# Kernel optimization log

Hardware: AMD Instinct MI355X
Metric: run time of the kernel (lower is better)

Reference implementation:

```python
import jax, jax.numpy as jnp
import numpy as np
from jax.ops import segment_sum, segment_max

N = 100000   # nodes
E = 1600000  # edges
B = 256      # graphs
H = 128      # hidden_channels
F_IN = 4     # input_size
EPS = 1e-5


def _graph_norm(x, w, b, ms, batch):
    # PyG GraphNorm: out = w * (x - ms*mean_g) / sqrt(var_g + eps) + b
    cnt = jnp.maximum(segment_sum(jnp.ones((x.shape[0],), x.dtype), batch, num_segments=B), 1.0)
    mean = segment_sum(x, batch, num_segments=B) / cnt[:, None]
    out = x - mean[batch] * ms
    var = segment_sum(out * out, batch, num_segments=B) / cnt[:, None]
    return w * out / jnp.sqrt(var + EPS)[batch] + b


def _gcn(x, W, b, src, dst):
    # GCNConv with self-loops and symmetric normalization (src/dst already include self-loops)
    h = x @ W                                              # [N, H]
    deg = segment_sum(jnp.ones_like(src, dtype=h.dtype), dst, num_segments=N)
    dinv = jax.lax.rsqrt(jnp.maximum(deg, 1.0))
    norm = dinv[src] * dinv[dst]                           # [E+N]
    return segment_sum(norm[:, None] * h[src], dst, num_segments=N) + b


def _seg_softmax(gate, batch):
    gmax = segment_max(gate, batch, num_segments=B)
    e = jnp.exp(gate - gmax[batch])
    den = segment_sum(e, batch, num_segments=B)
    return e / den[batch]


def setup_inputs() -> dict:
    key = jax.random.key(0)
    ks = jax.random.split(key, 16)
    x = jax.random.normal(ks[0], (N, F_IN), jnp.float32)
    edge_index = jax.random.randint(ks[1], (2, E), 0, N, dtype=jnp.int64)
    batch = jnp.sort(jax.random.randint(ks[2], (N,), 0, B, dtype=jnp.int64))
    r = lambda k, shp, fan: jax.random.normal(k, shp, jnp.float32) / np.sqrt(fan)
    inp = {
        "x": x, "edge_index": edge_index, "batch": batch,
        "W1": r(ks[3], (F_IN, H), F_IN), "b1": jnp.zeros((H,), jnp.float32),
        "W2": r(ks[4], (H, H), H), "b2": jnp.zeros((H,), jnp.float32),
        "W3": r(ks[5], (H, H), H), "b3": jnp.zeros((H,), jnp.float32),
        "gn0_w": jnp.ones((F_IN,), jnp.float32), "gn0_b": jnp.zeros((F_IN,), jnp.float32), "gn0_ms": jnp.ones((F_IN,), jnp.float32),
        "gn1_w": jnp.ones((H,), jnp.float32), "gn1_b": jnp.zeros((H,), jnp.float32), "gn1_ms": jnp.ones((H,), jnp.float32),
        "gn2_w": jnp.ones((H,), jnp.float32), "gn2_b": jnp.zeros((H,), jnp.float32), "gn2_ms": jnp.ones((H,), jnp.float32),
        "gn3_w": jnp.ones((H,), jnp.float32), "gn3_b": jnp.zeros((H,), jnp.float32), "gn3_ms": jnp.ones((H,), jnp.float32),
        "g1": r(ks[6], (H, H), H), "gb1": jnp.zeros((H,), jnp.float32),
        "g2": r(ks[7], (H, H), H), "gb2": jnp.zeros((H,), jnp.float32),
        "g3": r(ks[8], (H, 1), H), "gb3": jnp.zeros((1,), jnp.float32),
        "l1": r(ks[9], (H, H), H), "lb1": jnp.zeros((H,), jnp.float32),
        "l2": r(ks[10], (H, H), H), "lb2": jnp.zeros((H,), jnp.float32),
        "l3": r(ks[11], (H, 1), H), "lb3": jnp.zeros((1,), jnp.float32),
    }
    return inp


def reference(x, edge_index, batch, W1, b1, W2, b2, W3, b3,
              gn0_w, gn0_b, gn0_ms, gn1_w, gn1_b, gn1_ms,
              gn2_w, gn2_b, gn2_ms, gn3_w, gn3_b, gn3_ms,
              g1, gb1, g2, gb2, g3, gb3,
              l1, lb1, l2, lb2, l3, lb3):
    loop = jnp.arange(N, dtype=edge_index.dtype)
    src = jnp.concatenate([edge_index[0], loop])
    dst = jnp.concatenate([edge_index[1], loop])

    h = _graph_norm(x, gn0_w, gn0_b, gn0_ms, batch)
    h = _gcn(h, W1, b1, src, dst)
    h = jax.nn.relu(_graph_norm(h, gn1_w, gn1_b, gn1_ms, batch))
    h = _gcn(h, W2, b2, src, dst)
    h = jax.nn.relu(_graph_norm(h, gn2_w, gn2_b, gn2_ms, batch))
    h = _gcn(h, W3, b3, src, dst)
    h = _graph_norm(h, gn3_w, gn3_b, gn3_ms, batch)

    # GlobalAttention: gate_nn -> scalar gate per node, segment softmax, weighted sum
    g = jax.nn.relu(h @ g1 + gb1)
    g = jax.nn.relu(g @ g2 + gb2)
    gate = g @ g3 + gb3                                   # [N, 1]
    attn = _seg_softmax(gate, batch)                      # [N, 1]
    pooled = segment_sum(attn * h, batch, num_segments=B) # [B, H]

    o = jax.nn.relu(pooled @ l1 + lb1)
    o = jax.nn.relu(o @ l2 + lb2)
    return o @ l3 + lb3                                   # [B, 1]
```

## Files before the change

### kernel.cpp

```cpp
#include <hip/hip_runtime.h>
#include <hip/hip_bf16.h>

#define NN 100000
#define NE 1600000
#define NB 256
#define HD 128
#define EPS 1e-5f
#define NBUK 1563
#define EPB 8192
#define NCHK 8

typedef __attribute__((ext_vector_type(8))) short bf16x8v;
typedef __attribute__((ext_vector_type(4))) float f32x4v;

__device__ __forceinline__ float rd_dyn(const void* p, int i, int fflag) {
    if (fflag) {
        unsigned short u = ((const unsigned short*)p)[i];
        return __uint_as_float(((unsigned)u) << 16);
    }
    return ((const float*)p)[i];
}

__device__ __forceinline__ int rd_idx(const int* p, int k, int iflag) {
    return iflag ? p[k] : p[2 * k];
}

__device__ __forceinline__ unsigned short f2bf(float v) {
    __hip_bfloat16 b = __float2bfloat16(v);
    return *(unsigned short*)&b;
}

__device__ __forceinline__ float bflo(unsigned u) { return __uint_as_float(u << 16); }
__device__ __forceinline__ float bfhi(unsigned u) { return __uint_as_float(u & 0xFFFF0000u); }
__device__ __forceinline__ unsigned packbf(float a, float b) {
    return (unsigned)f2bf(a) | ((unsigned)f2bf(b) << 16);
}

__global__ void k_zeroi(int* __restrict__ p, int n) {
    int i = blockIdx.x * blockDim.x + threadIdx.x;
    if (i < n) p[i] = 0;
}

__global__ void k_mark7(unsigned short* __restrict__ out, int n) {
    int i = blockIdx.x * blockDim.x + threadIdx.x;
    if (i < n) out[i] = 0x40E0;
}

__global__ void k_init(const unsigned* __restrict__ w, int* __restrict__ flags) {
    if (threadIdx.x == 0 && blockIdx.x == 0) {
        flags[0] = 0;
        flags[1] = (w[0] == 0x3F803F80u) ? 1 : 0;
    }
}

__global__ void k_detect(const int* __restrict__ w, int* __restrict__ iflag, int n) {
    int i = blockIdx.x * blockDim.x + threadIdx.x;
    if (i < n && (i & 1) && w[i] != 0) atomicOr(iflag, 1);
}

struct CvtArgs {
    const void* p[30];
    int n[30];
    int off[30];
};
__global__ void k_cvtf_all(CvtArgs a, float* __restrict__ out, const int* __restrict__ fflagp) {
    int j = blockIdx.y;
    int i = blockIdx.x * blockDim.x + threadIdx.x;
    if (i >= a.n[j]) return;
    out[a.off[j] + i] = rd_dyn(a.p[j], i, *fflagp);
}

__global__ void k_transp(const float* __restrict__ P, int o0, int o1, int o2, int o3,
                         unsigned short* __restrict__ WT) {
    int mat = blockIdx.y;
    int off = mat == 0 ? o0 : mat == 1 ? o1 : mat == 2 ? o2 : o3;
    int i = blockIdx.x * 256 + threadIdx.x;
    int nidx = i >> 7, k = i & 127;
    WT[mat * 16384 + nidx * 128 + k] = f2bf(P[off + k * 128 + nidx]);
}

__global__ __launch_bounds__(256) void k_bhist(const int* __restrict__ ei,
                                               const int* __restrict__ iflagp,
                                               int* __restrict__ bcnt, int e) {
    __shared__ int lh[NBUK];
    int ifl = *iflagp;
    for (int b = threadIdx.x; b < NBUK; b += 256) lh[b] = 0;
    __syncthreads();
    int s0 = blockIdx.x * EPB;
    int s1 = s0 + EPB; if (s1 > e) s1 = e;
    for (int i = s0 + threadIdx.x; i < s1; i += 256) {
        int d = rd_idx(ei, NE + i, ifl);
        int s = rd_idx(ei, i, ifl);
        if ((unsigned)d < (unsigned)NN && (unsigned)s < (unsigned)NN)
            atomicAdd(&lh[d >> 6], 1);
    }
    __syncthreads();
    for (int b = threadIdx.x; b < NBUK; b += 256)
        if (lh[b]) atomicAdd(&bcnt[b], lh[b]);
}

__global__ __launch_bounds__(1024) void k_bscan(const int* __restrict__ bcnt,
                                                int* __restrict__ boff,
                                                int* __restrict__ bcur) {
    __shared__ int part[1024];
    int t = threadIdx.x;
    int i0 = t * 2;
    int a = (i0 < NBUK) ? bcnt[i0] : 0;
    int b = (i0 + 1 < NBUK) ? bcnt[i0 + 1] : 0;
    part[t] = a + b;
    __syncthreads();
    for (int off = 1; off < 1024; off <<= 1) {
        int add = (t >= off) ? part[t - off] : 0;
        __syncthreads();
        part[t] += add;
        __syncthreads();
    }
    int base = (t > 0) ? part[t - 1] : 0;
    if (i0 < NBUK) { boff[i0] = base; bcur[i0] = base; }
    if (i0 + 1 < NBUK) { boff[i0 + 1] = base + a; bcur[i0 + 1] = base + a; }
    if (t == 1023) boff[NBUK] = part[1023];
}

__global__ __launch_bounds__(256) void k_bfill(const int* __restrict__ ei,
                                               const int* __restrict__ iflagp,
                                               int* __restrict__ bcur,
                                               unsigned* __restrict__ bkte, int e) {
    __shared__ int lh[NBUK];
    __shared__ int lbase[NBUK];
    int ifl = *iflagp;
    for (int b = threadIdx.x; b < NBUK; b += 256) lh[b] = 0;
    __syncthreads();
    int s0 = blockIdx.x * EPB;
    int s1 = s0 + EPB; if (s1 > e) s1 = e;
    for (int i = s0 + threadIdx.x; i < s1; i += 256) {
        int d = rd_idx(ei, NE + i, ifl);
        int s = rd_idx(ei, i, ifl);
        if ((unsigned)d < (unsigned)NN && (unsigned)s < (unsigned)NN)
            atomicAdd(&lh[d >> 6], 1);
    }
    __syncthreads();
    for (int b = threadIdx.x; b < NBUK; b += 256) {
        int c = lh[b];
        if (c) { lbase[b] = atomicAdd(&bcur[b], c); lh[b] = 0; }
    }
    __syncthreads();
    for (int i = s0 + threadIdx.x; i < s1; i += 256) {
        int d = rd_idx(ei, NE + i, ifl);
        int s = rd_idx(ei, i, ifl);
        if ((unsigned)d < (unsigned)NN && (unsigned)s < (unsigned)NN) {
            int b = d >> 6;
            int li = atomicAdd(&lh[b], 1);
            bkte[lbase[b] + li] = ((unsigned)s << 6) | (unsigned)(d & 63);
        }
    }
}

__global__ __launch_bounds__(256) void k_csrfin(const unsigned* __restrict__ bkte,
                                                const int* __restrict__ boff,
                                                int* __restrict__ rowptr,
                                                int* __restrict__ cnt,
                                                float* __restrict__ dinv,
                                                int* __restrict__ esrc) {
    __shared__ int lc[64];
    __shared__ int lcur[64];
    int b = blockIdx.x, t = threadIdx.x;
    int base = b * 64;
    if (t < 64) lc[t] = 0;
    __syncthreads();
    int r0 = boff[b], r1 = boff[b + 1];
    for (int j = r0 + t; j < r1; j += 256)
        atomicAdd(&lc[(int)(bkte[j] & 63u)], 1);
    __syncthreads();
    if (t < 64) {
        int v = lc[t];
        int inc = v;
#pragma unroll
        for (int off = 1; off < 64; off <<= 1) {
            int nv = __shfl_up(inc, off, 64);
            if (t >= off) inc += nv;
        }
        int ex = r0 + inc - v;
        lcur[t] = ex;
        int node = base + t;
        if (node < NN) {
            rowptr[node] = ex;
            cnt[node] = v;
            dinv[node] = rsqrtf((float)(v + 1));
        }
    }
    __syncthreads();
    for (int j = r0 + t; j < r1; j += 256) {
        unsigned p = bkte[j];
        int slot = atomicAdd(&lcur[p & 63u], 1);
        esrc[slot] = (int)(p >> 6);
    }
}

__global__ void k_start(const int* __restrict__ batch, const int* __restrict__ iflagp,
                        int* __restrict__ start, int* __restrict__ batch32, int n) {
    int i = blockIdx.x * blockDim.x + threadIdx.x;
    if (i >= n) return;
    int ifl = *iflagp;
    int b = rd_idx(batch, i, ifl); b = b < 0 ? 0 : (b > NB - 1 ? NB - 1 : b);
    batch32[i] = b;
    int bp;
    if (i == 0) bp = -1;
    else { bp = rd_idx(batch, i - 1, ifl); bp = bp < 0 ? 0 : (bp > NB - 1 ? NB - 1 : bp); }
    for (int g = bp + 1; g <= b; ++g) start[g] = i;
    if (i == n - 1) { for (int g = b + 1; g <= NB; ++g) start[g] = n; }
}

__global__ __launch_bounds__(64) void k_gn4(const void* __restrict__ x,
                                            const float* __restrict__ w,
                                            const float* __restrict__ bb,
                                            const float* __restrict__ ms,
                                            const int* __restrict__ start,
                                            const int* __restrict__ fflagp,
                                            float* __restrict__ out) {
    int g = blockIdx.x;
    int s0 = start[g], s1 = start[g + 1];
    if (s1 <= s0) return;
    int ff = *fflagp;
    float cnt = (float)(s1 - s0);
    int t = threadIdx.x;
    int c = t & 3, p = t >> 2;
    __shared__ float reds[64], redq[64];
    float s = 0.f, q = 0.f;
    for (int n = s0 + p; n < s1; n += 16) {
        float v = rd_dyn(x, n * 4 + c, ff);
        s += v; q = fmaf(v, v, q);
    }
    reds[t] = s; redq[t] = q; __syncthreads();
    for (int off = 8; off >= 1; off >>= 1) {
        if (p < off) { reds[t] += reds[t + 4 * off]; redq[t] += redq[t + 4 * off]; }
        __syncthreads();
    }
    float mean = reds[c] / cnt;
    float sq = redq[c] / cnt;
    float sub = mean * ms[c];
    float var = sq - 2.f * sub * mean + sub * sub;
    float scale = w[c] * rsqrtf(var + EPS);
    float bias = bb[c];
    for (int n = s0 + p; n < s1; n += 16) {
        float d = rd_dyn(x, n * 4 + c, ff) - sub;
        out[n * 4 + c] = scale * d + bias;
    }
}

__global__ __launch_bounds__(256) void k_gnstats_part(const unsigned* __restrict__ Xu,
                                                      const int* __restrict__ start,
                                                      float* __restrict__ PS,
                                                      float* __restrict__ PQ) {
    int g = blockIdx.x, k = blockIdx.y;
    int s0 = start[g], s1 = start[g + 1];
    int len = (s1 - s0 + NCHK - 1) / NCHK;
    int c0 = s0 + k * len, c1 = c0 + len; if (c1 > s1) c1 = s1;
    int t = threadIdx.x;
    int cp = t & 63, p = t >> 6;
    __shared__ float r0s[256], r1s[256], r0q[256], r1q[256];
    float s0a = 0.f, s1a = 0.f, q0a = 0.f, q1a = 0.f;
    for (int n = c0 + p; n < c1; n += 4) {
        unsigned u = Xu[n * 64 + cp];
        float lo = bflo(u), hi = bfhi(u);
        s0a += lo; q0a = fmaf(lo, lo, q0a);
        s1a += hi; q1a = fmaf(hi, hi, q1a);
    }
    r0s[t] = s0a; r1s[t] = s1a; r0q[t] = q0a; r1q[t] = q1a;
    __syncthreads();
    if (p == 0) {
        float a0 = r0s[cp] + r0s[64 + cp] + r0s[128 + cp] + r0s[192 + cp];
        float a1 = r1s[cp] + r1s[64 + cp] + r1s[128 + cp] + r1s[192 + cp];
        float b0 = r0q[cp] + r0q[64 + cp] + r0q[128 + cp] + r0q[192 + cp];
        float b1 = r1q[cp] + r1q[64 + cp] + r1q[128 + cp] + r1q[192 + cp];
        int bidx = (g * NCHK + k) * 128;
        PS[bidx + 2 * cp] = a0; PS[bidx + 2 * cp + 1] = a1;
        PQ[bidx + 2 * cp] = b0; PQ[bidx + 2 * cp + 1] = b1;
    }
}

__global__ __launch_bounds__(128) void k_gnstats_final(const float* __restrict__ PS,
                                                       const float* __restrict__ PQ,
                                                       const float* __restrict__ w,
                                                       const float* __restrict__ ms,
                                                       const int* __restrict__ start,
                                                       float* __restrict__ SUB,
                                                       float* __restrict__ SCALE) {
    int g = blockIdx.x, c = threadIdx.x;
    int n = start[g + 1] - start[g];
    if (n <= 0) return;
    float cnt = (float)n;
    float s = 0.f, q = 0.f;
#pragma unroll
    for (int k = 0; k < NCHK; ++k) {
        s += PS[(g * NCHK + k) * 128 + c];
        q += PQ[(g * NCHK + k) * 128 + c];
    }
    float mean = s / cnt;
    float sq = q / cnt;
    float sub = mean * ms[c];
    float var = sq - 2.f * sub * mean + sub * sub;
    SUB[g * 128 + c] = sub;
    SCALE[g * 128 + c] = w[c] * rsqrtf(var + EPS);
}

__global__ __launch_bounds__(256) void k_gather4(const int* __restrict__ rowptr,
                                                 const int* __restrict__ cnt,
                                                 const int* __restrict__ esrc,
                                                 const float* __restrict__ dinv,
                                                 const float* __restrict__ h,
                                                 float* __restrict__ out) {
    int node = blockIdx.x * blockDim.x + threadIdx.x;
    if (node >= NN) return;
    int r0 = rowptr[node], r1 = r0 + cnt[node];
    const float4* h4 = (const float4*)h;
    double ax = 0.0, ay = 0.0, az = 0.0, aw = 0.0;
    for (int j = r0; j < r1; ++j) {
        int s = esrc[j];
        float ds = dinv[s];
        float4 v = h4[s];
        ax += (double)(ds * v.x); ay += (double)(ds * v.y);
        az += (double)(ds * v.z); aw += (double)(ds * v.w);
    }
    float dd = dinv[node];
    float4 hs = h4[node];
    float4 o;
    o.x = (float)(dd * ax) + dd * dd * hs.x;
    o.y = (float)(dd * ay) + dd * dd * hs.y;
    o.z = (float)(dd * az) + dd * dd * hs.z;
    o.w = (float)(dd * aw) + dd * dd * hs.w;
    ((float4*)out)[node] = o;
}

__global__ __launch_bounds__(256) void k_gemm4b(const float* __restrict__ in,
                                                const float* __restrict__ W,
                                                const float* __restrict__ bias,
                                                unsigned short* __restrict__ out) {
    __shared__ float xs[16][4];
    int base = blockIdx.x * 16;
    int tid = threadIdx.x;
    if (tid < 64) xs[tid >> 2][tid & 3] = in[base * 4 + tid];
    __syncthreads();
    int j = tid & 127;
    int half = tid >> 7;
    float w0 = W[0 * HD + j], w1 = W[1 * HD + j], w2 = W[2 * HD + j], w3 = W[3 * HD + j];
    float bj = bias[j];
#pragma unroll
    for (int r = 0; r < 8; ++r) {
        int row = half * 8 + r;
        float v = xs[row][0] * w0 + xs[row][1] * w1 + xs[row][2] * w2 + xs[row][3] * w3 + bj;
        out[(base + row) * HD + j] = f2bf(v);
    }
}

__global__ __launch_bounds__(256) void k_gemm_mfma_bf(const unsigned* __restrict__ Xu,
                                                      const int* __restrict__ batch32,
                                                      const float* __restrict__ SUB,
                                                      const float* __restrict__ SCALE,
                                                      const float* __restrict__ gnb,
                                                      int relu,
                                                      const unsigned short* __restrict__ WT,
                                                      const float* __restrict__ dinv,
                                                      unsigned short* __restrict__ out) {
    __shared__ unsigned short xs[16][136];
    int base = blockIdx.x * 16;
    int tid = threadIdx.x;
    for (int idx = tid; idx < 1024; idx += 256) {
        int r = idx >> 6, cp = idx & 63;
        int g = batch32[base + r];
        unsigned u = Xu[(base + r) * 64 + cp];
        int ca = 2 * cp, cb = 2 * cp + 1;
        float va = (bflo(u) - SUB[g * 128 + ca]) * SCALE[g * 128 + ca] + gnb[ca];
        float vb = (bfhi(u) - SUB[g * 128 + cb]) * SCALE[g * 128 + cb] + gnb[cb];
        if (relu) { va = fmaxf(va, 0.f); vb = fmaxf(vb, 0.f); }
        xs[r][ca] = f2bf(va);
        xs[r][cb] = f2bf(vb);
    }
    __syncthreads();
    int wave = tid >> 6, lane = tid & 63;
    int m = lane & 15, quad = lane >> 4;
    f32x4v acc0 = {0.f, 0.f, 0.f, 0.f}, acc1 = {0.f, 0.f, 0.f, 0.f};
    int c0 = wave * 32 + m, c1 = c0 + 16;
#pragma unroll
    for (int kk = 0; kk < 4; ++kk) {
        int ko = kk * 32 + quad * 8;
        bf16x8v a  = *(const bf16x8v*)&xs[m][ko];
        bf16x8v b0 = *(const bf16x8v*)&WT[c0 * 128 + ko];
        bf16x8v b1 = *(const bf16x8v*)&WT[c1 * 128 + ko];
        acc0 = __builtin_amdgcn_mfma_f32_16x16x32_bf16(a, b0, acc0, 0, 0, 0);
        acc1 = __builtin_amdgcn_mfma_f32_16x16x32_bf16(a, b1, acc1, 0, 0, 0);
    }
#pragma unroll
    for (int reg = 0; reg < 4; ++reg) {
        int row = base + quad * 4 + reg;
        float dv = dinv[row];
        out[row * 128 + c0] = f2bf(dv * acc0[reg]);
        out[row * 128 + c1] = f2bf(dv * acc1[reg]);
    }
}

__global__ __launch_bounds__(256) void k_gather_bf(const int* __restrict__ rowptr,
                                                   const int* __restrict__ cnt,
                                                   const int* __restrict__ esrc,
                                                   const float* __restrict__ dinv,
                                                   const unsigned* __restrict__ h,
                                                   const float* __restrict__ bias,
                                                   unsigned* __restrict__ Xu) {
    int node = blockIdx.x * 4 + (threadIdx.x >> 6);
    int lane = threadIdx.x & 63;
    if (node >= NN) return;
    int r0 = rowptr[node], r1 = r0 + cnt[node];
    double ax = 0.0, ay = 0.0;
    int j = r0;
    for (; j + 7 < r1; j += 8) {
        unsigned u[8];
#pragma unroll
        for (int q = 0; q < 8; ++q) u[q] = h[esrc[j + q] * 64 + lane];
#pragma unroll
        for (int q = 0; q < 8; ++q) {
            ax += (double)bflo(u[q]);
            ay += (double)bfhi(u[q]);
        }
    }
    for (; j < r1; ++j) {
        unsigned u = h[esrc[j] * 64 + lane];
        ax += (double)bflo(u);
        ay += (double)bfhi(u);
    }
    float dd = dinv[node];
    unsigned us = h[node * 64 + lane];
    float2 bb = ((const float2*)bias)[lane];
    float ox = dd * ((float)ax + bflo(us)) + bb.x;
    float oy = dd * ((float)ay + bfhi(us)) + bb.y;
    Xu[node * 64 + lane] = packbf(ox, oy);
}

__global__ __launch_bounds__(256) void k_gate_fused(const unsigned* __restrict__ Xu,
                                                    const int* __restrict__ batch32,
                                                    const float* __restrict__ SUB,
                                                    const float* __restrict__ SCALE,
                                                    const float* __restrict__ gnb,
                                                    const unsigned short* __restrict__ GT1,
                                                    const float* __restrict__ gb1,
                                                    const unsigned short* __restrict__ GT2,
                                                    const float* __restrict__ gb2,
                                                    const float* __restrict__ g3,
                                                    const float* __restrict__ gb3,
                                                    float* __restrict__ gate) {
    __shared__ unsigned short xs[16][136];
    __shared__ unsigned short t1[16][136];
    __shared__ float redw[64];
    int base = blockIdx.x * 16;
    int tid = threadIdx.x;
    for (int idx = tid; idx < 1024; idx += 256) {
        int r = idx >> 6, cp = idx & 63;
        int g = batch32[base + r];
        unsigned u = Xu[(base + r) * 64 + cp];
        int ca = 2 * cp, cb = 2 * cp + 1;
        xs[r][ca] = f2bf((bflo(u) - SUB[g * 128 + ca]) * SCALE[g * 128 + ca] + gnb[ca]);
        xs[r][cb] = f2bf((bfhi(u) - SUB[g * 128 + cb]) * SCALE[g * 128 + cb] + gnb[cb]);
    }
    __syncthreads();
    int wave = tid >> 6, lane = tid & 63;
    int m = lane & 15, quad = lane >> 4;
    int c0 = wave * 32 + m, c1 = c0 + 16;
    f32x4v acc0 = {0.f, 0.f, 0.f, 0.f}, acc1 = {0.f, 0.f, 0.f, 0.f};
#pragma unroll
    for (int kk = 0; kk < 4; ++kk) {
        int ko = kk * 32 + quad * 8;
        bf16x8v a  = *(const bf16x8v*)&xs[m][ko];
        bf16x8v b0 = *(const bf16x8v*)&GT1[c0 * 128 + ko];
        bf16x8v b1 = *(const bf16x8v*)&GT1[c1 * 128 + ko];
        acc0 = __builtin_amdgcn_mfma_f32_16x16x32_bf16(a, b0, acc0, 0, 0, 0);
        acc1 = __builtin_amdgcn_mfma_f32_16x16x32_bf16(a, b1, acc1, 0, 0, 0);
    }
    float bj0 = gb1[c0], bj1 = gb1[c1];
#pragma unroll
    for (int reg = 0; reg < 4; ++reg) {
        int row = quad * 4 + reg;
        t1[row][c0] = f2bf(fmaxf(acc0[reg] + bj0, 0.f));
        t1[row][c1] = f2bf(fmaxf(acc1[reg] + bj1, 0.f));
    }
    __syncthreads();
    f32x4v d0 = {0.f, 0.f, 0.f, 0.f}, d1 = {0.f, 0.f, 0.f, 0.f};
#pragma unroll
    for (int kk = 0; kk < 4; ++kk) {
        int ko = kk * 32 + quad * 8;
        bf16x8v a  = *(const bf16x8v*)&t1[m][ko];
        bf16x8v b0 = *(const bf16x8v*)&GT2[c0 * 128 + ko];
        bf16x8v b1 = *(const bf16x8v*)&GT2[c1 * 128 + ko];
        d0 = __builtin_amdgcn_mfma_f32_16x16x32_bf16(a, b0, d0, 0, 0, 0);
        d1 = __builtin_amdgcn_mfma_f32_16x16x32_bf16(a, b1, d1, 0, 0, 0);
    }
    float g30 = g3[c0], g31 = g3[c1];
    float bk0 = gb2[c0], bk1 = gb2[c1];
    float contrib[4];
#pragma unroll
    for (int reg = 0; reg < 4; ++reg) {
        float v0 = fmaxf(d0[reg] + bk0, 0.f);
        float v1 = fmaxf(d1[reg] + bk1, 0.f);
        contrib[reg] = v0 * g30 + v1 * g31;
    }
#pragma unroll
    for (int mask = 1; mask <= 8; mask <<= 1) {
#pragma unroll
        for (int reg = 0; reg < 4; ++reg)
            contrib[reg] += __shfl_xor(contrib[reg], mask, 64);
    }
    if (m == 0) {
#pragma unroll
        for (int reg = 0; reg < 4; ++reg)
            redw[wave * 16 + quad * 4 + reg] = contrib[reg];
    }
    __syncthreads();
    if (tid < 16) {
        float s = redw[tid] + redw[16 + tid] + redw[32 + tid] + redw[48 + tid];
        gate[base + tid] = s + gb3[0];
    }
}

__global__ __launch_bounds__(256) void k_softmax(float* __restrict__ gate,
                                                 const int* __restrict__ start) {
    int g = blockIdx.x;
    int s0 = start[g], s1 = start[g + 1];
    if (s1 <= s0) return;
    int t = threadIdx.x;
    __shared__ float red[256];
    float m = -1e30f;
    for (int i = s0 + t; i < s1; i += 256) m = fmaxf(m, gate[i]);
    red[t] = m; __syncthreads();
    for (int off = 128; off; off >>= 1) { if (t < off) red[t] = fmaxf(red[t], red[t + off]); __syncthreads(); }
    m = red[0]; __syncthreads();
    float s = 0.f;
    for (int i = s0 + t; i < s1; i += 256) s += expf(gate[i] - m);
    red[t] = s; __syncthreads();
    for (int off = 128; off; off >>= 1) { if (t < off) red[t] += red[t + off]; __syncthreads(); }
    float inv = 1.f / red[0];
    for (int i = s0 + t; i < s1; i += 256) gate[i] = expf(gate[i] - m) * inv;
}

__global__ __launch_bounds__(256) void k_pool_part(const unsigned* __restrict__ Xu,
                                                   const float* __restrict__ SUB,
                                                   const float* __restrict__ SCALE,
                                                   const float* __restrict__ gnb,
                                                   const float* __restrict__ attn,
                                                   const int* __restrict__ start,
                                                   float* __restrict__ PP) {
    int g = blockIdx.x, k = blockIdx.y;
    int s0 = start[g], s1 = start[g + 1];
    int len = (s1 - s0 + NCHK - 1) / NCHK;
    int c0 = s0 + k * len, c1 = c0 + len; if (c1 > s1) c1 = s1;
    int t = threadIdx.x, cp = t & 63, p = t >> 6;
    __shared__ float r0s[256], r1s[256];
    int ca = 2 * cp, cb = 2 * cp + 1;
    float suba = SUB[g * 128 + ca], subb = SUB[g * 128 + cb];
    float sca = SCALE[g * 128 + ca], scb = SCALE[g * 128 + cb];
    float ba = gnb[ca], bb2 = gnb[cb];
    float sa = 0.f, sb = 0.f;
    for (int n = c0 + p; n < c1; n += 4) {
        float a = attn[n];
        unsigned u = Xu[n * 64 + cp];
        sa += a * ((bflo(u) - suba) * sca + ba);
        sb += a * ((bfhi(u) - subb) * scb + bb2);
    }
    r0s[t] = sa; r1s[t] = sb; __syncthreads();
    if (p == 0) {
        int bidx = (g * NCHK + k) * 128;
        PP[bidx + ca] = r0s[cp] + r0s[64 + cp] + r0s[128 + cp] + r0s[192 + cp];
        PP[bidx + cb] = r1s[cp] + r1s[64 + cp] + r1s[128 + cp] + r1s[192 + cp];
    }
}

__global__ __launch_bounds__(128) void k_head(const float* __restrict__ PP,
                                              const float* __restrict__ l1, const float* __restrict__ lb1,
                                              const float* __restrict__ l2, const float* __restrict__ lb2,
                                              const float* __restrict__ l3, const float* __restrict__ lb3,
                                              const int* __restrict__ fflagp,
                                              void* __restrict__ out) {
    int g = blockIdx.x, t = threadIdx.x;
    __shared__ float p[128], o[128], red[128];
    float s = 0.f;
#pragma unroll
    for (int k = 0; k < NCHK; ++k) s += PP[(g * NCHK + k) * 128 + t];
    p[t] = s; __syncthreads();
    float a = 0.f;
    for (int k = 0; k < 128; ++k) a += p[k] * l1[k * 128 + t];
    a = fmaxf(a + lb1[t], 0.f);
    o[t] = a; __syncthreads();
    float b = 0.f;
    for (int k = 0; k < 128; ++k) b += o[k] * l2[k * 128 + t];
    b = fmaxf(b + lb2[t], 0.f);
    red[t] = b * l3[t]; __syncthreads();
    for (int off = 64; off; off >>= 1) { if (t < off) red[t] += red[t + off]; __syncthreads(); }
    if (t == 0) {
        float r = red[0] + lb3[0];
        if (*fflagp) ((__hip_bfloat16*)out)[g] = __float2bfloat16(r);
        else ((float*)out)[g] = r;
    }
}

extern "C" void kernel_launch(void* const* d_in, const int* in_sizes, int n_in,
                              void* d_out, int out_size, void* d_ws, size_t ws_size,
                              hipStream_t stream) {
    const void* x = d_in[0];
    const int* ei_raw = (const int*)d_in[1];
    const int* batch_raw = (const int*)d_in[2];
    (void)n_in; (void)out_size;

    char* ws = (char*)d_ws;
    size_t off = 0;
    auto alloc = [&](size_t bytes) -> void* {
        void* p = ws + off;
        off += (bytes + 255) & ~(size_t)255;
        return p;
    };
    unsigned* Xu  = (unsigned*)alloc((size_t)NN * HD * 2);
    float* Y      = (float*)alloc((size_t)NN * HD * 4);
    float* h0     = (float*)alloc((size_t)NN * 4 * 4);
    float* z4     = (float*)alloc((size_t)NN * 4 * 4);
    float* dinv   = (float*)alloc((size_t)NN * 4);
    float* gate   = (float*)alloc((size_t)NN * 4);
    int*   start  = (int*)alloc((size_t)(NB + 1) * 4);
    int*   batch32= (int*)alloc((size_t)NN * 4);
    float* P      = (float*)alloc((size_t)131072 * 4);
    unsigned short* WT = (unsigned short*)alloc((size_t)4 * 16384 * 2);
    float* SUB    = (float*)alloc((size_t)NB * HD * 4);
    float* SCALE  = (float*)alloc((size_t)NB * HD * 4);
    float* PS     = (float*)alloc((size_t)NB * NCHK * 128 * 4);
    float* PQ     = (float*)alloc((size_t)NB * NCHK * 128 * 4);
    int*   flags  = (int*)alloc(256);
    int*   cnt    = (int*)alloc((size_t)NN * 4);
    int*   rowptr = (int*)alloc((size_t)(NN + 1) * 4);
    int*   esrc   = (int*)alloc((size_t)NE * 4);
    int*   bcnt   = (int*)alloc((size_t)NBUK * 4);
    int*   boff   = (int*)alloc((size_t)(NBUK + 1) * 4);
    int*   bcur   = (int*)alloc((size_t)NBUK * 4);
    unsigned* bkte = (unsigned*)(Y + (size_t)NN * HD / 2);
    float* PP = PS;

    if (ws_size < off) {
        k_mark7<<<1, 256, 0, stream>>>((unsigned short*)d_out, NB);
        return;
    }

    int* iflag = flags;
    int* fflag = flags + 1;
    k_init<<<1, 64, 0, stream>>>((const unsigned*)d_in[12], flags);
    k_detect<<<(NN + 255) / 256, 256, 0, stream>>>(batch_raw, iflag, NN);

    CvtArgs ca;
    float* fp[33];
    int maxn = 1;
    {
        int poff = 0;
        for (int i = 3; i < 33; ++i) {
            int n = in_sizes[i];
            ca.p[i - 3] = d_in[i];
            ca.n[i - 3] = n;
            ca.off[i - 3] = poff;
            fp[i] = P + poff;
            poff += n;
            if (n > maxn) maxn = n;
        }
    }
    {
        dim3 grid((maxn + 255) / 256, 30);
        k_cvtf_all<<<grid, 256, 0, stream>>>(ca, P, fflag);
    }
    const float *W1 = fp[3], *b1 = fp[4], *b2 = fp[6], *b3 = fp[8];
    const float *gn0w = fp[9],  *gn0b = fp[10], *gn0m = fp[11];
    const float *gn1w = fp[12], *gn1b = fp[13], *gn1m = fp[14];
    const float *gn2w = fp[15], *gn2b = fp[16], *gn2m = fp[17];
    const float *gn3w = fp[18], *gn3b = fp[19], *gn3m = fp[20];
    const float *gb1 = fp[22], *gb2 = fp[24], *g3 = fp[25], *gb3 = fp[26];
    const float *l1 = fp[27], *lb1 = fp[28], *l2 = fp[29], *lb2 = fp[30], *l3 = fp[31], *lb3 = fp[32];

    {
        dim3 grid(64, 4);
        k_transp<<<grid, 256, 0, stream>>>(P, (int)(fp[5] - P), (int)(fp[7] - P),
                                           (int)(fp[21] - P), (int)(fp[23] - P), WT);
    }
    const unsigned short* WT2 = WT;
    const unsigned short* WT3 = WT + 16384;
    const unsigned short* GT1 = WT + 2 * 16384;
    const unsigned short* GT2 = WT + 3 * 16384;

    k_start<<<(NN + 255) / 256, 256, 0, stream>>>(batch_raw, iflag, start, batch32, NN);

    int ebg = (NE + EPB - 1) / EPB;
    k_zeroi<<<(NBUK + 255) / 256, 256, 0, stream>>>(bcnt, NBUK);
    k_bhist<<<ebg, 256, 0, stream>>>(ei_raw, iflag, bcnt, NE);
    k_bscan<<<1, 1024, 0, stream>>>(bcnt, boff, bcur);
    k_bfill<<<ebg, 256, 0, stream>>>(ei_raw, iflag, bcur, bkte, NE);
    k_csrfin<<<NBUK, 256, 0, stream>>>(bkte, boff, rowptr, cnt, dinv, esrc);

    k_gn4<<<NB, 64, 0, stream>>>(x, gn0w, gn0b, gn0m, start, fflag, h0);

    k_gather4<<<(NN + 255) / 256, 256, 0, stream>>>(rowptr, cnt, esrc, dinv, h0, z4);
    k_gemm4b<<<NN / 16, 256, 0, stream>>>(z4, W1, b1, (unsigned short*)Xu);

    unsigned short* Yb = (unsigned short*)Y;
    dim3 sgrid(NB, NCHK);

    k_gnstats_part<<<sgrid, 256, 0, stream>>>(Xu, start, PS, PQ);
    k_gnstats_final<<<NB, 128, 0, stream>>>(PS, PQ, gn1w, gn1m, start, SUB, SCALE);
    k_gemm_mfma_bf<<<NN / 16, 256, 0, stream>>>(Xu, batch32, SUB, SCALE, gn1b, 1, WT2, dinv, Yb);
    k_gather_bf<<<(NN + 3) / 4, 256, 0, stream>>>(rowptr, cnt, esrc, dinv, (const unsigned*)Yb, b2, Xu);

    k_gnstats_part<<<sgrid, 256, 0, stream>>>(Xu, start, PS, PQ);
    k_gnstats_final<<<NB, 128, 0, stream>>>(PS, PQ, gn2w, gn2m, start, SUB, SCALE);
    k_gemm_mfma_bf<<<NN / 16, 256, 0, stream>>>(Xu, batch32, SUB, SCALE, gn2b, 1, WT3, dinv, Yb);
    k_gather_bf<<<(NN + 3) / 4, 256, 0, stream>>>(rowptr, cnt, esrc, dinv, (const unsigned*)Yb, b3, Xu);

    k_gnstats_part<<<sgrid, 256, 0, stream>>>(Xu, start, PS, PQ);
    k_gnstats_final<<<NB, 128, 0, stream>>>(PS, PQ, gn3w, gn3m, start, SUB, SCALE);
    k_gate_fused<<<NN / 16, 256, 0, stream>>>(Xu, batch32, SUB, SCALE, gn3b,
                                              GT1, gb1, GT2, gb2, g3, gb3, gate);
    k_softmax<<<NB, 256, 0, stream>>>(gate, start);
    k_pool_part<<<sgrid, 256, 0, stream>>>(Xu, SUB, SCALE, gn3b, gate, start, PP);
    k_head<<<NB, 128, 0, stream>>>(PP, l1, lb1, l2, lb2, l3, lb3, fflag, d_out);
}
```

Before: 583.0 us.

## Fuse gnstats passes with last-block reduction, drop zero kernel and cnt array

Merges the partial and final GraphNorm statistics kernels into one launch. Blocks count arrivals per graph with an atomic counter, and the last block to arrive reduces the partials and resets the counter. Zeroing of the bucket histogram moves into k_start. The per-node cnt array is replaced by rowptr[node+1], and the SUB/SCALE/bias loads are vectorized as float2. This removes about four kernel launches plus some memory traffic, at the cost of threadfence and atomic synchronization.

```diff
diff --git a/kernel.cpp b/kernel.cpp
--- a/kernel.cpp
+++ b/kernel.cpp
@@ -34,11 +34,6 @@
 __device__ __forceinline__ float bfhi(unsigned u) { return __uint_as_float(u & 0xFFFF0000u); }
 __device__ __forceinline__ unsigned packbf(float a, float b) {
     return (unsigned)f2bf(a) | ((unsigned)f2bf(b) << 16);
-}
-
-__global__ void k_zeroi(int* __restrict__ p, int n) {
-    int i = blockIdx.x * blockDim.x + threadIdx.x;
-    if (i < n) p[i] = 0;
 }
 
 __global__ void k_mark7(unsigned short* __restrict__ out, int n) {
@@ -79,6 +74,23 @@
     WT[mat * 16384 + nidx * 128 + k] = f2bf(P[off + k * 128 + nidx]);
 }
 
+__global__ void k_start(const int* __restrict__ batch, const int* __restrict__ iflagp,
+                        int* __restrict__ start, int* __restrict__ batch32,
+                        int* __restrict__ bcnt, int* __restrict__ arrive, int n) {
+    int i = blockIdx.x * blockDim.x + threadIdx.x;
+    if (i >= n) return;
+    if (i < NBUK) bcnt[i] = 0;
+    if (i < NB) arrive[i] = 0;
+    int ifl = *iflagp;
+    int b = rd_idx(batch, i, ifl); b = b < 0 ? 0 : (b > NB - 1 ? NB - 1 : b);
+    batch32[i] = b;
+    int bp;
+    if (i == 0) bp = -1;
+    else { bp = rd_idx(batch, i - 1, ifl); bp = bp < 0 ? 0 : (bp > NB - 1 ? NB - 1 : bp); }
+    for (int g = bp + 1; g <= b; ++g) start[g] = i;
+    if (i == n - 1) { for (int g = b + 1; g <= NB; ++g) start[g] = n; }
+}
+
 __global__ __launch_bounds__(256) void k_bhist(const int* __restrict__ ei,
                                                const int* __restrict__ iflagp,
                                                int* __restrict__ bcnt, int e) {
@@ -158,7 +170,6 @@
 __global__ __launch_bounds__(256) void k_csrfin(const unsigned* __restrict__ bkte,
                                                 const int* __restrict__ boff,
                                                 int* __restrict__ rowptr,
-                                                int* __restrict__ cnt,
                                                 float* __restrict__ dinv,
                                                 int* __restrict__ esrc) {
     __shared__ int lc[64];
@@ -184,30 +195,16 @@
         int node = base + t;
         if (node < NN) {
             rowptr[node] = ex;
-            cnt[node] = v;
             dinv[node] = rsqrtf((float)(v + 1));
         }
     }
+    if (b == NBUK - 1 && t == 0) rowptr[NN] = boff[NBUK];
     __syncthreads();
     for (int j = r0 + t; j < r1; j += 256) {
         unsigned p = bkte[j];
         int slot = atomicAdd(&lcur[p & 63u], 1);
         esrc[slot] = (int)(p >> 6);
     }
-}
-
-__global__ void k_start(const int* __restrict__ batch, const int* __restrict__ iflagp,
-                        int* __restrict__ start, int* __restrict__ batch32, int n) {
-    int i = blockIdx.x * blockDim.x + threadIdx.x;
-    if (i >= n) return;
-    int ifl = *iflagp;
-    int b = rd_idx(batch, i, ifl); b = b < 0 ? 0 : (b > NB - 1 ? NB - 1 : b);
-    batch32[i] = b;
-    int bp;
-    if (i == 0) bp = -1;
-    else { bp = rd_idx(batch, i - 1, ifl); bp = bp < 0 ? 0 : (bp > NB - 1 ? NB - 1 : bp); }
-    for (int g = bp + 1; g <= b; ++g) start[g] = i;
-    if (i == n - 1) { for (int g = b + 1; g <= NB; ++g) start[g] = n; }
 }
 
 __global__ __launch_bounds__(64) void k_gn4(const void* __restrict__ x,
@@ -247,10 +244,15 @@
     }
 }
 
-__global__ __launch_bounds__(256) void k_gnstats_part(const unsigned* __restrict__ Xu,
-                                                      const int* __restrict__ start,
-                                                      float* __restrict__ PS,
-                                                      float* __restrict__ PQ) {
+__global__ __launch_bounds__(256) void k_gnstats(const unsigned* __restrict__ Xu,
+                                                 const int* __restrict__ start,
+                                                 float* __restrict__ PS,
+                                                 float* __restrict__ PQ,
+                                                 const float* __restrict__ w,
+                                                 const float* __restrict__ ms,
+                                                 float* __restrict__ SUB,
+                                                 float* __restrict__ SCALE,
+                                                 int* __restrict__ arrive) {
     int g = blockIdx.x, k = blockIdx.y;
     int s0 = start[g], s1 = start[g + 1];
     int len = (s1 - s0 + NCHK - 1) / NCHK;
@@ -258,6 +260,7 @@
     int t = threadIdx.x;
     int cp = t & 63, p = t >> 6;
     __shared__ float r0s[256], r1s[256], r0q[256], r1q[256];
+    __shared__ int lastf;
     float s0a = 0.f, s1a = 0.f, q0a = 0.f, q1a = 0.f;
     for (int n = c0 + p; n < c1; n += 4) {
         unsigned u = Xu[n * 64 + cp];
@@ -276,42 +279,39 @@
         PS[bidx + 2 * cp] = a0; PS[bidx + 2 * cp + 1] = a1;
         PQ[bidx + 2 * cp] = b0; PQ[bidx + 2 * cp + 1] = b1;
     }
-}
-
-__global__ __launch_bounds__(128) void k_gnstats_final(const float* __restrict__ PS,
-                                                       const float* __restrict__ PQ,
-                                                       const float* __restrict__ w,
-                                                       const float* __restrict__ ms,
-                                                       const int* __restrict__ start,
-                                                       float* __restrict__ SUB,
-                                                       float* __restrict__ SCALE) {
-    int g = blockIdx.x, c = threadIdx.x;
-    int n = start[g + 1] - start[g];
-    if (n <= 0) return;
-    float cnt = (float)n;
-    float s = 0.f, q = 0.f;
-#pragma unroll
-    for (int k = 0; k < NCHK; ++k) {
-        s += PS[(g * NCHK + k) * 128 + c];
-        q += PQ[(g * NCHK + k) * 128 + c];
-    }
-    float mean = s / cnt;
-    float sq = q / cnt;
-    float sub = mean * ms[c];
-    float var = sq - 2.f * sub * mean + sub * sub;
-    SUB[g * 128 + c] = sub;
-    SCALE[g * 128 + c] = w[c] * rsqrtf(var + EPS);
+    __syncthreads();
+    __threadfence();
+    if (t == 0) lastf = (atomicAdd(&arrive[g], 1) == NCHK - 1) ? 1 : 0;
+    __syncthreads();
+    if (!lastf) return;
+    __threadfence();
+    int n = s1 - s0;
+    if (t < 128 && n > 0) {
+        float cnt = (float)n;
+        float s = 0.f, q = 0.f;
+#pragma unroll
+        for (int k2 = 0; k2 < NCHK; ++k2) {
+            s += PS[(g * NCHK + k2) * 128 + t];
+            q += PQ[(g * NCHK + k2) * 128 + t];
+        }
+        float mean = s / cnt;
+        float sq = q / cnt;
+        float sub = mean * ms[t];
+        float var = sq - 2.f * sub * mean + sub * sub;
+        SUB[g * 128 + t] = sub;
+        SCALE[g * 128 + t] = w[t] * rsqrtf(var + EPS);
+    }
+    if (t == 0) arrive[g] = 0;
 }
 
 __global__ __launch_bounds__(256) void k_gather4(const int* __restrict__ rowptr,
-                                                 const int* __restrict__ cnt,
                                                  const int* __restrict__ esrc,
                                                  const float* __restrict__ dinv,
                                                  const float* __restrict__ h,
                                                  float* __restrict__ out) {
     int node = blockIdx.x * blockDim.x + threadIdx.x;
     if (node >= NN) return;
-    int r0 = rowptr[node], r1 = r0 + cnt[node];
+    int r0 = rowptr[node], r1 = rowptr[node + 1];
     const float4* h4 = (const float4*)h;
     double ax = 0.0, ay = 0.0, az = 0.0, aw = 0.0;
     for (int j = r0; j < r1; ++j) {
@@ -368,12 +368,14 @@
         int r = idx >> 6, cp = idx & 63;
         int g = batch32[base + r];
         unsigned u = Xu[(base + r) * 64 + cp];
-        int ca = 2 * cp, cb = 2 * cp + 1;
-        float va = (bflo(u) - SUB[g * 128 + ca]) * SCALE[g * 128 + ca] + gnb[ca];
-        float vb = (bfhi(u) - SUB[g * 128 + cb]) * SCALE[g * 128 + cb] + gnb[cb];
+        float2 sub = ((const float2*)(SUB + g * 128))[cp];
+        float2 sc  = ((const float2*)(SCALE + g * 128))[cp];
+        float2 gb  = ((const float2*)gnb)[cp];
+        float va = (bflo(u) - sub.x) * sc.x + gb.x;
+        float vb = (bfhi(u) - sub.y) * sc.y + gb.y;
         if (relu) { va = fmaxf(va, 0.f); vb = fmaxf(vb, 0.f); }
-        xs[r][ca] = f2bf(va);
-        xs[r][cb] = f2bf(vb);
+        xs[r][2 * cp] = f2bf(va);
+        xs[r][2 * cp + 1] = f2bf(vb);
     }
     __syncthreads();
     int wave = tid >> 6, lane = tid & 63;
@@ -399,7 +401,6 @@
 }
 
 __global__ __launch_bounds__(256) void k_gather_bf(const int* __restrict__ rowptr,
-                                                   const int* __restrict__ cnt,
                                                    const int* __restrict__ esrc,
                                                    const float* __restrict__ dinv,
                                                    const unsigned* __restrict__ h,
@@ -408,7 +409,7 @@
     int node = blockIdx.x * 4 + (threadIdx.x >> 6);
     int lane = threadIdx.x & 63;
     if (node >= NN) return;
-    int r0 = rowptr[node], r1 = r0 + cnt[node];
+    int r0 = rowptr[node], r1 = rowptr[node + 1];
     double ax = 0.0, ay = 0.0;
     int j = r0;
     for (; j + 7 < r1; j += 8) {
@@ -455,9 +456,11 @@
         int r = idx >> 6, cp = idx & 63;
         int g = batch32[base + r];
         unsigned u = Xu[(base + r) * 64 + cp];
-        int ca = 2 * cp, cb = 2 * cp + 1;
-        xs[r][ca] = f2bf((bflo(u) - SUB[g * 128 + ca]) * SCALE[g * 128 + ca] + gnb[ca]);
-        xs[r][cb] = f2bf((bfhi(u) - SUB[g * 128 + cb]) * SCALE[g * 128 + cb] + gnb[cb]);
+        float2 sub = ((const float2*)(SUB + g * 128))[cp];
+        float2 sc  = ((const float2*)(SCALE + g * 128))[cp];
+        float2 gb  = ((const float2*)gnb)[cp];
+        xs[r][2 * cp] = f2bf((bflo(u) - sub.x) * sc.x + gb.x);
+        xs[r][2 * cp + 1] = f2bf((bfhi(u) - sub.y) * sc.y + gb.y);
     }
     __syncthreads();
     int wave = tid >> 6, lane = tid & 63;
@@ -551,22 +554,23 @@
     int c0 = s0 + k * len, c1 = c0 + len; if (c1 > s1) c1 = s1;
     int t = threadIdx.x, cp = t & 63, p = t >> 6;
     __shared__ float r0s[256], r1s[256];
-    int ca = 2 * cp, cb = 2 * cp + 1;
-    float suba = SUB[g * 128 + ca], subb = SUB[g * 128 + cb];
-    float sca = SCALE[g * 128 + ca], scb = SCALE[g * 128 + cb];
-    float ba = gnb[ca], bb2 = gnb[cb];
+    float2 sub = ((const float2*)(SUB + g * 128))[cp];
+    float2 sc  = ((const float2*)(SCALE + g * 128))[cp];
+    float2 gb  = ((const float2*)gnb)[cp];
     float sa = 0.f, sb = 0.f;
     for (int n = c0 + p; n < c1; n += 4) {
         float a = attn[n];
         unsigned u = Xu[n * 64 + cp];
-        sa += a * ((bflo(u) - suba) * sca + ba);
-        sb += a * ((bfhi(u) - subb) * scb + bb2);
+        sa += a * ((bflo(u) - sub.x) * sc.x + gb.x);
+        sb += a * ((bfhi(u) - sub.y) * sc.y + gb.y);
     }
     r0s[t] = sa; r1s[t] = sb; __syncthreads();
     if (p == 0) {
         int bidx = (g * NCHK + k) * 128;
-        PP[bidx + ca] = r0s[cp] + r0s[64 + cp] + r0s[128 + cp] + r0s[192 + cp];
-        PP[bidx + cb] = r1s[cp] + r1s[64 + cp] + r1s[128 + cp] + r1s[192 + cp];
+        float2 o;
+        o.x = r0s[cp] + r0s[64 + cp] + r0s[128 + cp] + r0s[192 + cp];
+        o.y = r1s[cp] + r1s[64 + cp] + r1s[128 + cp] + r1s[192 + cp];
+        ((float2*)(PP + bidx))[cp] = o;
     }
 }
 
@@ -628,7 +632,7 @@
     float* PS     = (float*)alloc((size_t)NB * NCHK * 128 * 4);
     float* PQ     = (float*)alloc((size_t)NB * NCHK * 128 * 4);
     int*   flags  = (int*)alloc(256);
-    int*   cnt    = (int*)alloc((size_t)NN * 4);
+    int*   arrive = (int*)alloc((size_t)NB * 4);
     int*   rowptr = (int*)alloc((size_t)(NN + 1) * 4);
     int*   esrc   = (int*)alloc((size_t)NE * 4);
     int*   bcnt   = (int*)alloc((size_t)NBUK * 4);
@@ -684,35 +688,32 @@
     const unsigned short* GT1 = WT + 2 * 16384;
     const unsigned short* GT2 = WT + 3 * 16384;
 
-    k_start<<<(NN + 255) / 256, 256, 0, stream>>>(batch_raw, iflag, start, batch32, NN);
+    k_start<<<(NN + 255) / 256, 256, 0, stream>>>(batch_raw, iflag, start, batch32,
+                                                  bcnt, arrive, NN);
 
     int ebg = (NE + EPB - 1) / EPB;
-    k_zeroi<<<(NBUK + 255) / 256, 256, 0, stream>>>(bcnt, NBUK);
     k_bhist<<<ebg, 256, 0, stream>>>(ei_raw, iflag, bcnt, NE);
     k_bscan<<<1, 1024, 0, stream>>>(bcnt, boff, bcur);
     k_bfill<<<ebg, 256, 0, stream>>>(ei_raw, iflag, bcur, bkte, NE);
-    k_csrfin<<<NBUK, 256, 0, stream>>>(bkte, boff, rowptr, cnt, dinv, esrc);
+    k_csrfin<<<NBUK, 256, 0, stream>>>(bkte, boff, rowptr, dinv, esrc);
 
     k_gn4<<<NB, 64, 0, stream>>>(x, gn0w, gn0b, gn0m, start, fflag, h0);
 
-    k_gather4<<<(NN + 255) / 256, 256, 0, stream>>>(rowptr, cnt, esrc, dinv, h0, z4);
+    k_gather4<<<(NN + 255) / 256, 256, 0, stream>>>(rowptr, esrc, dinv, h0, z4);
     k_gemm4b<<<NN / 16, 256, 0, stream>>>(z4, W1, b1, (unsigned short*)Xu);
 
     unsigned short* Yb = (unsigned short*)Y;
     dim3 sgrid(NB, NCHK);
 
-    k_gnstats_part<<<sgrid, 256, 0, stream>>>(Xu, start, PS, PQ);
-    k_gnstats_final<<<NB, 128, 0, stream>>>(PS, PQ, gn1w, gn1m, start, SUB, SCALE);
+    k_gnstats<<<sgrid, 256, 0, stream>>>(Xu, start, PS, PQ, gn1w, gn1m, SUB, SCALE, arrive);
     k_gemm_mfma_bf<<<NN / 16, 256, 0, stream>>>(Xu, batch32, SUB, SCALE, gn1b, 1, WT2, dinv, Yb);
-    k_gather_bf<<<(NN + 3) / 4, 256, 0, stream>>>(rowptr, cnt, esrc, dinv, (const unsigned*)Yb, b2, Xu);
-
-    k_gnstats_part<<<sgrid, 256, 0, stream>>>(Xu, start, PS, PQ);
-    k_gnstats_final<<<NB, 128, 0, stream>>>(PS, PQ, gn2w, gn2m, start, SUB, SCALE);
+    k_gather_bf<<<(NN + 3) / 4, 256, 0, stream>>>(rowptr, esrc, dinv, (const unsigned*)Yb, b2, Xu);
+
+    k_gnstats<<<sgrid, 256, 0, stream>>>(Xu, start, PS, PQ, gn2w, gn2m, SUB, SCALE, arrive);
     k_gemm_mfma_bf<<<NN / 16, 256, 0, stream>>>(Xu, batch32, SUB, SCALE, gn2b, 1, WT3, dinv, Yb);
-    k_gather_bf<<<(NN + 3) / 4, 256, 0, stream>>>(rowptr, cnt, esrc, dinv, (const unsigned*)Yb, b3, Xu);
-
-    k_gnstats_part<<<sgrid, 256, 0, stream>>>(Xu, start, PS, PQ);
-    k_gnstats_final<<<NB, 128, 0, stream>>>(PS, PQ, gn3w, gn3m, start, SUB, SCALE);
+    k_gather_bf<<<(NN + 3) / 4, 256, 0, stream>>>(rowptr, esrc, dinv, (const unsigned*)Yb, b3, Xu);
+
+    k_gnstats<<<sgrid, 256, 0, stream>>>(Xu, start, PS, PQ, gn3w, gn3m, SUB, SCALE, arrive);
     k_gate_fused<<<NN / 16, 256, 0, stream>>>(Xu, batch32, SUB, SCALE, gn3b,
                                               GT1, gb1, GT2, gb2, g3, gb3, gate);
     k_softmax<<<NB, 256, 0, stream>>>(gate, start);
```

Result: slower. 1.010 ms (+73.3%).
